# Optimization experiments

Measured on AMD Instinct MI355X. Metric: run time of the kernel, lower is better.

The kernel has to match this reference:

```python
import jax, jax.numpy as jnp
import numpy as np

N_POINTS = 4_000_000   # total points in batch
N_PROPOSALS = 4096     # number of proposals
MIN_NPOINT = 256       # test_cfg.min_npoint: fixed slice length per proposal


def setup_inputs() -> dict:
    key = jax.random.key(0)
    k1, k2, k3 = jax.random.split(key, 3)
    semantic_scores = jax.random.normal(k1, (N_POINTS, 2), dtype=jnp.float32)
    pt_offsets = jax.random.normal(k2, (N_POINTS, 3), dtype=jnp.float32)
    # proposals_idx: column 0 = proposal id, column 1 = point index into [0, N)
    point_ids = jax.random.randint(k3, (N_PROPOSALS * MIN_NPOINT,), 0, N_POINTS, dtype=jnp.int32)
    prop_ids = jnp.repeat(jnp.arange(N_PROPOSALS, dtype=jnp.int32), MIN_NPOINT)
    proposals_idx = jnp.stack([prop_ids, point_ids], axis=1)  # [T, 2]
    # cumulative offsets; every proposal here has exactly MIN_NPOINT points
    proposals_offset = (jnp.arange(N_PROPOSALS + 1, dtype=jnp.int32) * MIN_NPOINT)
    return {
        "semantic_scores": semantic_scores,
        "proposals_offset": proposals_offset,
        "proposals_idx": proposals_idx,
        "pt_offsets": pt_offsets,
        "min_npoint": MIN_NPOINT,
    }


def reference(semantic_scores, proposals_offset, proposals_idx, pt_offsets, min_npoint):
    """Vectorized get_offset_4feats: per-proposal [mean, median, min, max] of
    ||pt_offsets[idx]|| over the first min_npoint indices of each proposal."""
    starts = proposals_offset[:-1]                                  # [P]
    gather = starts[:, None] + jnp.arange(min_npoint)[None, :]      # [P, K]
    prop_ind = proposals_idx[gather, 1]                             # [P, K] point indices
    radius = jnp.linalg.norm(pt_offsets[prop_ind], axis=-1)        # [P, K]
    srt = jnp.sort(radius, axis=1)                                  # one sort gives median/min/max
    mean = jnp.mean(radius, axis=1)
    median = srt[:, (min_npoint - 1) // 2]  # torch.median = lower middle for even K
    off_feats = jnp.stack([mean, median, srt[:, 0], srt[:, -1]], axis=1)  # [P, 4]
    return off_feats.astype(semantic_scores.dtype)
```

## Files before the change

### kernel.cpp

```cpp
#include <hip/hip_runtime.h>
#include <math.h>

__global__ __launch_bounds__(256) void offs4feat_kernel(
    const int*   __restrict__ prop_offset,
    const int*   __restrict__ prop_idx,
    const float* __restrict__ pt_offsets,
    const int*   __restrict__ npoint_ptr,
    float*       __restrict__ out)
{
    __shared__ float sh[256];
    __shared__ float wsum[4];

    const int p  = blockIdx.x;
    const int t  = threadIdx.x;
    const int np = *npoint_ptr;
    const int start = prop_offset[p];

    const bool active = (t < np);
    float radius = INFINITY;
    if (active) {
        const int idx = prop_idx[(size_t)(start + t) * 2 + 1];
        const float x = pt_offsets[(size_t)idx * 3 + 0];
        const float y = pt_offsets[(size_t)idx * 3 + 1];
        const float z = pt_offsets[(size_t)idx * 3 + 2];
        radius = sqrtf(fmaf(x, x, fmaf(y, y, z * z)));
    }

    float s = active ? radius : 0.0f;
    #pragma unroll
    for (int off = 32; off > 0; off >>= 1)
        s += __shfl_down(s, off, 64);
    const int wave = t >> 6;
    if ((t & 63) == 0) wsum[wave] = s;

    float v = radius;
    #pragma unroll
    for (int k = 2; k <= 256; k <<= 1) {
        #pragma unroll
        for (int j = k >> 1; j >= 64; j >>= 1) {
            __syncthreads();
            sh[t] = v;
            __syncthreads();
            const float o = sh[t ^ j];
            const bool keep_min = (((t & k) == 0) == ((t & j) == 0));
            v = keep_min ? fminf(v, o) : fmaxf(v, o);
        }
        #pragma unroll
        for (int j = (k >> 1) < 32 ? (k >> 1) : 32; j >= 1; j >>= 1) {
            const float o = __shfl_xor(v, j, 64);
            const bool keep_min = (((t & k) == 0) == ((t & j) == 0));
            v = keep_min ? fminf(v, o) : fmaxf(v, o);
        }
    }

    __syncthreads();

    if (t == 0) {
        float S = 0.0f;
        const int nw = (blockDim.x + 63) >> 6;
        for (int w = 0; w < nw; ++w) S += wsum[w];
        out[p * 4 + 0] = S / (float)np;
        out[p * 4 + 2] = v;
    }
    if (t == (np - 1) / 2) out[p * 4 + 1] = v;
    if (t == np - 1)       out[p * 4 + 3] = v;
}

extern "C" void kernel_launch(void* const* d_in, const int* in_sizes, int n_in,
                              void* d_out, int out_size, void* d_ws, size_t ws_size,
                              hipStream_t stream) {
    const int*   prop_offset = (const int*)  d_in[1];
    const int*   prop_idx    = (const int*)  d_in[2];
    const float* pt_offsets  = (const float*)d_in[3];
    const int*   npoint_ptr  = (const int*)  d_in[4];
    float*       out         = (float*)      d_out;

    const int n_proposals = in_sizes[1] - 1;

    offs4feat_kernel<<<n_proposals, 256, 0, stream>>>(
        prop_offset, prop_idx, pt_offsets, npoint_ptr, out);
}
```

Baseline: 27.96 us.

## Sort each proposal within one wavefront using 4 elements per lane

Each 64-lane wavefront now handles a whole proposal, with every lane holding 4 radii in registers. The bitonic sort runs as in-register compare-exchanges plus cross-lane shuffles, so the shared-memory stages and block-wide barriers go away. Blocks carry four proposals each, and the index loads become int2 vector reads. The cost is more registers per thread, and the kernel now handles at most 256 points per proposal.

```diff
diff --git a/kernel.cpp b/kernel.cpp
--- a/kernel.cpp
+++ b/kernel.cpp
@@ -1,69 +1,115 @@
 #include <hip/hip_runtime.h>
 #include <math.h>
+
+
+#define CX_LANE(K, J)                                                         \
+    {                                                                         \
+        const int  ls       = (J) >> 2;                                       \
+        const bool keep_min = (((e0 & (K)) == 0) == ((e0 & (J)) == 0));       \
+        _Pragma("unroll")                                                     \
+        for (int r = 0; r < 4; ++r) {                                         \
+            const float o  = __shfl_xor(v[r], ls, 64);                        \
+            const float mn = fminf(v[r], o);                                  \
+            const float mx = fmaxf(v[r], o);                                  \
+            v[r] = keep_min ? mn : mx;                                        \
+        }                                                                     \
+    }
+
+#define CX_REG2(K)                                                            \
+    {                                                                         \
+        const bool a = ((e0 & (K)) == 0);                                     \
+        float mn = fminf(v[0], v[2]), mx = fmaxf(v[0], v[2]);                 \
+        v[0] = a ? mn : mx; v[2] = a ? mx : mn;                               \
+        mn = fminf(v[1], v[3]); mx = fmaxf(v[1], v[3]);                       \
+        v[1] = a ? mn : mx; v[3] = a ? mx : mn;                               \
+    }
+
+#define CX_REG1(K)                                                            \
+    {                                                                         \
+        const bool a01 = (((e0 + 0) & (K)) == 0);                             \
+        const bool a23 = (((e0 + 2) & (K)) == 0);                             \
+        float mn = fminf(v[0], v[1]), mx = fmaxf(v[0], v[1]);                 \
+        v[0] = a01 ? mn : mx; v[1] = a01 ? mx : mn;                           \
+        mn = fminf(v[2], v[3]); mx = fmaxf(v[2], v[3]);                       \
+        v[2] = a23 ? mn : mx; v[3] = a23 ? mx : mn;                           \
+    }
 
 __global__ __launch_bounds__(256) void offs4feat_kernel(
     const int*   __restrict__ prop_offset,
     const int*   __restrict__ prop_idx,
     const float* __restrict__ pt_offsets,
     const int*   __restrict__ npoint_ptr,
-    float*       __restrict__ out)
+    float*       __restrict__ out,
+    int n_props)
 {
-    __shared__ float sh[256];
-    __shared__ float wsum[4];
+    const int t    = threadIdx.x;
+    const int lane = t & 63;
+    const int p    = blockIdx.x * 4 + (t >> 6);
+    if (p >= n_props) return;
 
-    const int p  = blockIdx.x;
-    const int t  = threadIdx.x;
-    const int np = *npoint_ptr;
+    const int np    = *npoint_ptr;
     const int start = prop_offset[p];
+    const int e0    = lane << 2;
 
-    const bool active = (t < np);
-    float radius = INFINITY;
-    if (active) {
-        const int idx = prop_idx[(size_t)(start + t) * 2 + 1];
-        const float x = pt_offsets[(size_t)idx * 3 + 0];
-        const float y = pt_offsets[(size_t)idx * 3 + 1];
-        const float z = pt_offsets[(size_t)idx * 3 + 2];
-        radius = sqrtf(fmaf(x, x, fmaf(y, y, z * z)));
-    }
-
-    float s = active ? radius : 0.0f;
-    #pragma unroll
-    for (int off = 32; off > 0; off >>= 1)
-        s += __shfl_down(s, off, 64);
-    const int wave = t >> 6;
-    if ((t & 63) == 0) wsum[wave] = s;
-
-    float v = radius;
-    #pragma unroll
-    for (int k = 2; k <= 256; k <<= 1) {
+    int id[4];
+    if (e0 + 3 < np) {
+        const int* base = prop_idx + (size_t)(start + e0) * 2;
+        const int2 a = *(const int2*)(base + 0);
+        const int2 b = *(const int2*)(base + 2);
+        const int2 c = *(const int2*)(base + 4);
+        const int2 d = *(const int2*)(base + 6);
+        id[0] = a.y; id[1] = b.y; id[2] = c.y; id[3] = d.y;
+    } else {
         #pragma unroll
-        for (int j = k >> 1; j >= 64; j >>= 1) {
-            __syncthreads();
-            sh[t] = v;
-            __syncthreads();
-            const float o = sh[t ^ j];
-            const bool keep_min = (((t & k) == 0) == ((t & j) == 0));
-            v = keep_min ? fminf(v, o) : fmaxf(v, o);
-        }
-        #pragma unroll
-        for (int j = (k >> 1) < 32 ? (k >> 1) : 32; j >= 1; j >>= 1) {
-            const float o = __shfl_xor(v, j, 64);
-            const bool keep_min = (((t & k) == 0) == ((t & j) == 0));
-            v = keep_min ? fminf(v, o) : fmaxf(v, o);
+        for (int r = 0; r < 4; ++r) {
+            int ei = e0 + r; ei = (ei < np) ? ei : (np - 1);
+            id[r] = prop_idx[(size_t)(start + ei) * 2 + 1];
         }
     }
 
-    __syncthreads();
+    float x[4], y[4], z[4];
+    #pragma unroll
+    for (int r = 0; r < 4; ++r) {
+        const float* q = pt_offsets + (size_t)id[r] * 3;
+        x[r] = q[0]; y[r] = q[1]; z[r] = q[2];
+    }
 
-    if (t == 0) {
-        float S = 0.0f;
-        const int nw = (blockDim.x + 63) >> 6;
-        for (int w = 0; w < nw; ++w) S += wsum[w];
-        out[p * 4 + 0] = S / (float)np;
-        out[p * 4 + 2] = v;
+    float v[4];
+    float s = 0.0f;
+    #pragma unroll
+    for (int r = 0; r < 4; ++r) {
+        const float rr = sqrtf(fmaf(x[r], x[r], fmaf(y[r], y[r], z[r] * z[r])));
+        const bool act = (e0 + r) < np;
+        s   += act ? rr : 0.0f;
+        v[r] = act ? rr : INFINITY;
     }
-    if (t == (np - 1) / 2) out[p * 4 + 1] = v;
-    if (t == np - 1)       out[p * 4 + 3] = v;
+
+    #pragma unroll
+    for (int o = 32; o > 0; o >>= 1) s += __shfl_xor(s, o, 64);
+
+    CX_REG1(2)
+    CX_REG2(4)  CX_REG1(4)
+    CX_LANE(8, 4)   CX_REG2(8)   CX_REG1(8)
+    CX_LANE(16, 8)  CX_LANE(16, 4)  CX_REG2(16)  CX_REG1(16)
+    CX_LANE(32, 16) CX_LANE(32, 8)  CX_LANE(32, 4)  CX_REG2(32)  CX_REG1(32)
+    CX_LANE(64, 32) CX_LANE(64, 16) CX_LANE(64, 8)  CX_LANE(64, 4)
+    CX_REG2(64)  CX_REG1(64)
+    CX_LANE(128, 64) CX_LANE(128, 32) CX_LANE(128, 16) CX_LANE(128, 8)
+    CX_LANE(128, 4)  CX_REG2(128) CX_REG1(128)
+    CX_LANE(256, 128) CX_LANE(256, 64) CX_LANE(256, 32) CX_LANE(256, 16)
+    CX_LANE(256, 8)   CX_LANE(256, 4)  CX_REG2(256) CX_REG1(256)
+
+    const int emed = (np - 1) >> 1;
+    const int emax = np - 1;
+    auto pick = [&](int rr_) {
+        return rr_ == 0 ? v[0] : rr_ == 1 ? v[1] : rr_ == 2 ? v[2] : v[3];
+    };
+    if (lane == 0) {
+        out[p * 4 + 0] = s / (float)np;
+        out[p * 4 + 2] = v[0];
+    }
+    if (lane == (emed >> 2)) out[p * 4 + 1] = pick(emed & 3);
+    if (lane == (emax >> 2)) out[p * 4 + 3] = pick(emax & 3);
 }
 
 extern "C" void kernel_launch(void* const* d_in, const int* in_sizes, int n_in,
@@ -76,7 +122,8 @@
     float*       out         = (float*)      d_out;
 
     const int n_proposals = in_sizes[1] - 1;
+    const int n_blocks    = (n_proposals + 3) / 4;
 
-    offs4feat_kernel<<<n_proposals, 256, 0, stream>>>(
-        prop_offset, prop_idx, pt_offsets, npoint_ptr, out);
+    offs4feat_kernel<<<n_blocks, 256, 0, stream>>>(
+        prop_offset, prop_idx, pt_offsets, npoint_ptr, out, n_proposals);
 }
```

Result: slower. 28.73 us (+2.7%).
